# Kernel tuning notes

Measured on AMD Instinct MI355X. Metric: run time of the kernel, lower is better.

Reference implementation:

```python
import jax, jax.numpy as jnp
import numpy as np

NEG_SLOPE = 0.2  # PyG GATConv default negative_slope
EPS = 1e-16     # PyG softmax denominator epsilon


def gat_conv(x, src, dst, W, a_src, a_dst, bias):
    """PyG GATConv (concat=True, dropout off). x:[N,Fin], src/dst:[E]."""
    N = x.shape[0]
    H, C = a_src.shape
    h = (x @ W).reshape(N, H, C)                      # per-head projected features
    es = jnp.einsum('nhc,hc->nh', h, a_src)           # alpha_src per node/head
    ed = jnp.einsum('nhc,hc->nh', h, a_dst)           # alpha_dst per node/head
    e = jax.nn.leaky_relu(es[src] + ed[dst], NEG_SLOPE)   # [E,H] edge scores
    # segment softmax over destination nodes (every node has a self loop)
    m = jax.ops.segment_max(e, dst, num_segments=N)
    p = jnp.exp(e - m[dst])
    denom = jax.ops.segment_sum(p, dst, num_segments=N)
    alpha = p / (denom[dst] + EPS)                    # [E,H]
    out = jax.ops.segment_sum(h[src] * alpha[:, :, None], dst, num_segments=N)
    return out.reshape(N, H * C) + bias


def _single_graph(x, ei, W1, a_src1, a_dst1, b1, W2, a_src2, a_dst2, b2):
    N = x.shape[0]
    loop = jnp.arange(N, dtype=ei.dtype)              # add_self_loops=True
    src = jnp.concatenate([ei[0], loop])
    dst = jnp.concatenate([ei[1], loop])
    h = jax.nn.relu(gat_conv(x, src, dst, W1, a_src1, a_dst1, b1))
    # F.dropout with p=0.0 is identity
    return gat_conv(h, src, dst, W2, a_src2, a_dst2, b2)


def setup_inputs() -> dict:
    key = jax.random.key(0)
    ks = jax.random.split(key, 9)
    B, N, E, F_in, H, C = 2, 20000, 320000, 128, 8, 64

    def glorot(k, shape):
        fan_in, fan_out = shape[-2] if len(shape) > 1 else shape[-1], shape[-1]
        s = np.sqrt(6.0 / (fan_in + fan_out)).astype(np.float32)
        return jax.random.uniform(k, shape, jnp.float32, -s, s)

    return {
        'xs': jax.random.normal(ks[0], (B, N, F_in), jnp.float32),
        'edge_indexs': jax.random.randint(ks[1], (B, 2, E), 0, N, jnp.int32),
        'W1': glorot(ks[2], (F_in, H * C)),
        'a_src1': glorot(ks[3], (H, C)),
        'a_dst1': glorot(ks[4], (H, C)),
        'b1': jnp.zeros((H * C,), jnp.float32),
        'W2': glorot(ks[5], (H * C, C)),
        'a_src2': glorot(ks[6], (1, C)),
        'a_dst2': glorot(ks[7], (1, C)),
        'b2': jnp.zeros((C,), jnp.float32),
    }


def reference(xs, edge_indexs, W1, a_src1, a_dst1, b1, W2, a_src2, a_dst2, b2):
    f = lambda x, ei: _single_graph(x, ei, W1, a_src1, a_dst1, b1, W2, a_src2, a_dst2, b2)
    return jax.vmap(f)(xs, edge_indexs)               # [B, N, C]
```

## Files before the change

kernel.cpp:

```cpp
#include <hip/hip_runtime.h>
#include <hip/hip_bf16.h>
#include <cstdint>

#define NEG_SLOPE 0.2f
#define SOFTMAX_EPS 1e-16f
#define NN 20000
#define EE 320000
#define CAP 48

typedef __hip_bfloat16 bf16;
typedef unsigned short ushort;
typedef short s8v __attribute__((ext_vector_type(8)));
typedef float f4v __attribute__((ext_vector_type(4)));
typedef float f2v __attribute__((ext_vector_type(2)));

static __device__ __forceinline__ float lo16(unsigned u) { return __uint_as_float(u << 16); }
static __device__ __forceinline__ float hi16(unsigned u) { return __uint_as_float(u & 0xffff0000u); }
static __device__ __forceinline__ ushort f2bf(float v) {
    bf16 h = __float2bfloat16(v);
    return *(ushort*)&h;
}

__global__ void prep_kernel(const float* __restrict__ W1, const float* __restrict__ W2,
                            const float* __restrict__ xs,
                            ushort* __restrict__ w1hi, ushort* __restrict__ w1lo,
                            ushort* __restrict__ w2hi, ushort* __restrict__ w2lo,
                            ushort* __restrict__ xhi, ushort* __restrict__ xlo,
                            int* __restrict__ count) {
    int bid = blockIdx.x;
    int t = threadIdx.x;
    if (bid >= 205) {
        size_t idx = (size_t)(bid - 205) * 2048 + (size_t)t * 8;
        float4 A = *(const float4*)&xs[idx];
        float4 B = *(const float4*)&xs[idx + 4];
        float v[8] = {A.x, A.y, A.z, A.w, B.x, B.y, B.z, B.w};
        unsigned hp[4], lp[4];
#pragma unroll
        for (int p = 0; p < 4; ++p) {
            ushort h0 = f2bf(v[p * 2]), h1 = f2bf(v[p * 2 + 1]);
            float l0 = v[p * 2] - __uint_as_float((unsigned)h0 << 16);
            float l1 = v[p * 2 + 1] - __uint_as_float((unsigned)h1 << 16);
            hp[p] = (unsigned)h0 | ((unsigned)h1 << 16);
            lp[p] = (unsigned)f2bf(l0) | ((unsigned)f2bf(l1) << 16);
        }
        *(uint4*)&xhi[idx] = make_uint4(hp[0], hp[1], hp[2], hp[3]);
        *(uint4*)&xlo[idx] = make_uint4(lp[0], lp[1], lp[2], lp[3]);
        return;
    }
    if (bid >= 48) {
        int idx = (bid - 48) * 256 + t;
        if (idx < 2 * NN) count[idx] = 0;
        return;
    }
    __shared__ float T[32][65];
    const float* src; ushort *dhi, *dlo; int K, C, c0, k0;
    if (bid < 32) { src = W1; dhi = w1hi; dlo = w1lo; K = 128; C = 512; c0 = (bid & 7) * 64; k0 = (bid >> 3) * 32; }
    else          { src = W2; dhi = w2hi; dlo = w2lo; K = 512; C = 64;  c0 = 0;              k0 = (bid - 32) * 32; }
    for (int i = 0; i < 8; ++i) {
        int flat = t + i * 256;
        int k = flat >> 6, c = flat & 63;
        T[k][c] = src[(size_t)(k0 + k) * C + c0 + c];
    }
    __syncthreads();
    int c = t >> 2, j0 = (t & 3) * 8;
    unsigned hp[4], lp[4];
#pragma unroll
    for (int p = 0; p < 4; ++p) {
        float v0 = T[j0 + p * 2][c], v1 = T[j0 + p * 2 + 1][c];
        ushort h0 = f2bf(v0), h1 = f2bf(v1);
        float l0 = v0 - __uint_as_float((unsigned)h0 << 16);
        float l1 = v1 - __uint_as_float((unsigned)h1 << 16);
        hp[p] = (unsigned)h0 | ((unsigned)h1 << 16);
        lp[p] = (unsigned)f2bf(l0) | ((unsigned)f2bf(l1) << 16);
    }
    size_t o = (size_t)(c0 + c) * K + k0 + j0;
    *(uint4*)&dhi[o] = make_uint4(hp[0], hp[1], hp[2], hp[3]);
    *(uint4*)&dlo[o] = make_uint4(lp[0], lp[1], lp[2], lp[3]);
}

#define G1S 40
static __device__ void gemm1_body(int b, int rem,
        const ushort* __restrict__ xhi, const ushort* __restrict__ xlo,
        const ushort* __restrict__ w1hi, const ushort* __restrict__ w1lo,
        const float* __restrict__ a_src, const float* __restrict__ a_dst,
        bf16* __restrict__ h1, float* __restrict__ es, float* __restrict__ ed) {
    __shared__ ushort lds[25600];
    int t = threadIdx.x;
    ushort* Xhi = lds;
    ushort* Xlo = lds + 2560;
    ushort* Whi = lds + 5120;
    ushort* Wlo = lds + 15360;
    int w = t >> 6, lane = t & 63, quad = lane >> 4, l16 = lane & 15;
    int nhalf = rem / 313;
    int row0 = (rem % 313) * 64, nbase = nhalf * 256;
    const ushort* xh = xhi + (size_t)b * NN * 128;
    const ushort* xl = xlo + (size_t)b * NN * 128;
    bf16*  h1b = h1 + (size_t)b * NN * 512;
    float* esb = es + (size_t)b * NN * 8;
    float* edb = ed + (size_t)b * NN * 8;

    f4v acc[16];
#pragma unroll
    for (int i = 0; i < 16; ++i) acc[i] = (f4v)0.f;

    for (int kc = 0; kc < 4; ++kc) {
        __syncthreads();
        {
            int row = t >> 2, c0 = (t & 3) * 8;
            uint4 hv, lv;
            if (row0 + row < NN) {
                size_t off = (size_t)(row0 + row) * 128 + kc * 32 + c0;
                hv = *(const uint4*)&xh[off];
                lv = *(const uint4*)&xl[off];
            } else { hv = make_uint4(0, 0, 0, 0); lv = hv; }
            *(uint4*)&Xhi[row * G1S + c0] = hv;
            *(uint4*)&Xlo[row * G1S + c0] = lv;
        }
        {
            const ushort* sh = w1hi + (size_t)(nbase + t) * 128 + kc * 32;
            const ushort* sl = w1lo + (size_t)(nbase + t) * 128 + kc * 32;
            uint4 h0 = *(const uint4*)(sh), h1_ = *(const uint4*)(sh + 8);
            uint4 h2 = *(const uint4*)(sh + 16), h3 = *(const uint4*)(sh + 24);
            uint4 l0 = *(const uint4*)(sl), l1 = *(const uint4*)(sl + 8);
            uint4 l2 = *(const uint4*)(sl + 16), l3 = *(const uint4*)(sl + 24);
            *(uint4*)&Whi[t * G1S]      = h0; *(uint4*)&Whi[t * G1S + 8]  = h1_;
            *(uint4*)&Whi[t * G1S + 16] = h2; *(uint4*)&Whi[t * G1S + 24] = h3;
            *(uint4*)&Wlo[t * G1S]      = l0; *(uint4*)&Wlo[t * G1S + 8]  = l1;
            *(uint4*)&Wlo[t * G1S + 16] = l2; *(uint4*)&Wlo[t * G1S + 24] = l3;
        }
        __syncthreads();
        int arow = (w * 16 + l16) * G1S + quad * 8;
        s8v ahi = *(const s8v*)&Xhi[arow];
        s8v alo = *(const s8v*)&Xlo[arow];
#pragma unroll
        for (int ct = 0; ct < 16; ++ct) {
            int baddr = (ct * 16 + l16) * G1S + quad * 8;
            s8v bhi = *(const s8v*)&Whi[baddr];
            s8v blo = *(const s8v*)&Wlo[baddr];
            acc[ct] = __builtin_amdgcn_mfma_f32_16x16x32_bf16(ahi, bhi, acc[ct], 0, 0, 0);
            acc[ct] = __builtin_amdgcn_mfma_f32_16x16x32_bf16(ahi, blo, acc[ct], 0, 0, 0);
            acc[ct] = __builtin_amdgcn_mfma_f32_16x16x32_bf16(alo, bhi, acc[ct], 0, 0, 0);
        }
    }

#pragma unroll
    for (int hh = 0; hh < 4; ++hh) {
        float s4[4] = {0.f, 0.f, 0.f, 0.f}, d4[4] = {0.f, 0.f, 0.f, 0.f};
#pragma unroll
        for (int ct4 = 0; ct4 < 4; ++ct4) {
            int ct = hh * 4 + ct4;
            int c = nbase + ct * 16 + l16;
            float as = a_src[c], ad = a_dst[c];
#pragma unroll
            for (int r = 0; r < 4; ++r) { s4[r] += acc[ct][r] * as; d4[r] += acc[ct][r] * ad; }
        }
#pragma unroll
        for (int o = 1; o < 16; o <<= 1) {
#pragma unroll
            for (int r = 0; r < 4; ++r) {
                s4[r] += __shfl_xor(s4[r], o);
                d4[r] += __shfl_xor(d4[r], o);
            }
        }
        if (l16 == 0) {
            int head = nhalf * 4 + hh;
#pragma unroll
            for (int r = 0; r < 4; ++r) {
                int gr = row0 + w * 16 + quad * 4 + r;
                if (gr < NN) { esb[gr * 8 + head] = s4[r]; edb[gr * 8 + head] = d4[r]; }
            }
        }
    }

    __syncthreads();
    ushort* rp = lds + w * 4224;
#pragma unroll
    for (int ct = 0; ct < 16; ++ct)
#pragma unroll
        for (int r = 0; r < 4; ++r)
            rp[(quad * 4 + r) * 264 + ct * 16 + l16] = f2bf(acc[ct][r]);
#pragma unroll
    for (int i = 0; i < 8; ++i) {
        int idx = i * 512 + lane * 8;
        int row = idx >> 8, col = idx & 255;
        uint4 vv = *(const uint4*)&rp[row * 264 + col];
        int gr = row0 + w * 16 + row;
        if (gr < NN) *(uint4*)&h1b[(size_t)gr * 512 + nbase + col] = vv;
    }
}

static __device__ void scatter_body(int idx, const int* __restrict__ ei,
                                    int* __restrict__ count, ushort* __restrict__ esrc) {
    int t = threadIdx.x;
    int b = idx / 1250;
    int e = (idx % 1250) * 256 + t;
    const int* srcA = ei + (size_t)b * 2 * EE;
    int s = srcA[e], d = srcA[EE + e];
    if ((unsigned)d >= NN || (unsigned)s >= NN) return;
    int pos = atomicAdd(&count[b * NN + d], 1);
    if (pos < CAP)
        esrc[((size_t)b * NN + d) * CAP + pos] = (ushort)s;
}

__global__ __launch_bounds__(256) void gemm1_scatter(
        const ushort* __restrict__ xhi, const ushort* __restrict__ xlo,
        const ushort* __restrict__ w1hi, const ushort* __restrict__ w1lo,
        const float* __restrict__ a_src, const float* __restrict__ a_dst,
        bf16* __restrict__ h1, float* __restrict__ es, float* __restrict__ ed,
        const int* __restrict__ ei, int* __restrict__ count, ushort* __restrict__ esrc) {
    int bid = blockIdx.x;
    if (bid < 1252) gemm1_body(bid / 626, bid % 626, xhi, xlo, w1hi, w1lo, a_src, a_dst, h1, es, ed);
    else            scatter_body(bid - 1252, ei, count, esrc);
}

#define G2S 72
__global__ __launch_bounds__(256) void gemm2_mfma(
        const bf16* __restrict__ a, const ushort* __restrict__ w2hi,
        const ushort* __restrict__ w2lo, const float* __restrict__ a_src,
        const float* __restrict__ a_dst, bf16* __restrict__ h2,
        float* __restrict__ es, float* __restrict__ ed) {
    __shared__ ushort lds2[13824];
    ushort* AS  = lds2;
    ushort* Whi = lds2 + 4608;
    ushort* Wlo = lds2 + 9216;

    int t = threadIdx.x;
    int w = t >> 6, lane = t & 63, quad = lane >> 4, l16 = lane & 15;
    int b = blockIdx.y;
    int row0 = blockIdx.x * 64;
    const bf16* ab = a + (size_t)b * NN * 512;
    bf16*  h2b = h2 + (size_t)b * NN * 512;
    float* esb = es + (size_t)b * NN;
    float* edb = ed + (size_t)b * NN;

    f4v acc[4];
#pragma unroll
    for (int i = 0; i < 4; ++i) acc[i] = (f4v)0.f;

    for (int kc = 0; kc < 8; ++kc) {
        __syncthreads();
        {
            int row = t >> 2, k0 = (t & 3) * 16;
            uint4 q0, q1;
            if (row0 + row < NN) {
                q0 = *(const uint4*)(ab + (size_t)(row0 + row) * 512 + kc * 64 + k0);
                q1 = *(const uint4*)(ab + (size_t)(row0 + row) * 512 + kc * 64 + k0 + 8);
            } else { q0 = make_uint4(0, 0, 0, 0); q1 = q0; }
            *(uint4*)&AS[row * G2S + k0]     = q0;
            *(uint4*)&AS[row * G2S + k0 + 8] = q1;
            const ushort* sh = w2hi + (size_t)row * 512 + kc * 64 + k0;
            const ushort* sl = w2lo + (size_t)row * 512 + kc * 64 + k0;
            *(uint4*)&Whi[row * G2S + k0]     = *(const uint4*)(sh);
            *(uint4*)&Whi[row * G2S + k0 + 8] = *(const uint4*)(sh + 8);
            *(uint4*)&Wlo[row * G2S + k0]     = *(const uint4*)(sl);
            *(uint4*)&Wlo[row * G2S + k0 + 8] = *(const uint4*)(sl + 8);
        }
        __syncthreads();
#pragma unroll
        for (int ks = 0; ks < 2; ++ks) {
            s8v av = *(const s8v*)&AS[(w * 16 + l16) * G2S + ks * 32 + quad * 8];
#pragma unroll
            for (int ct = 0; ct < 4; ++ct) {
                int baddr = (ct * 16 + l16) * G2S + ks * 32 + quad * 8;
                s8v bhi = *(const s8v*)&Whi[baddr];
                s8v blo = *(const s8v*)&Wlo[baddr];
                acc[ct] = __builtin_amdgcn_mfma_f32_16x16x32_bf16(av, bhi, acc[ct], 0, 0, 0);
                acc[ct] = __builtin_amdgcn_mfma_f32_16x16x32_bf16(av, blo, acc[ct], 0, 0, 0);
            }
        }
    }

    {
        float s4[4] = {0.f, 0.f, 0.f, 0.f}, d4[4] = {0.f, 0.f, 0.f, 0.f};
#pragma unroll
        for (int ct = 0; ct < 4; ++ct) {
            int c = ct * 16 + l16;
            float as = a_src[c], ad = a_dst[c];
#pragma unroll
            for (int r = 0; r < 4; ++r) { s4[r] += acc[ct][r] * as; d4[r] += acc[ct][r] * ad; }
        }
#pragma unroll
        for (int o = 1; o < 16; o <<= 1) {
#pragma unroll
            for (int r = 0; r < 4; ++r) {
                s4[r] += __shfl_xor(s4[r], o);
                d4[r] += __shfl_xor(d4[r], o);
            }
        }
        if (l16 == 0) {
#pragma unroll
            for (int r = 0; r < 4; ++r) {
                int gr = row0 + w * 16 + quad * 4 + r;
                if (gr < NN) { esb[gr] = s4[r]; edb[gr] = d4[r]; }
            }
        }
    }

    __syncthreads();
    ushort* rp = lds2 + w * 1152;
#pragma unroll
    for (int ct = 0; ct < 4; ++ct)
#pragma unroll
        for (int r = 0; r < 4; ++r)
            rp[(quad * 4 + r) * G2S + ct * 16 + l16] = f2bf(acc[ct][r]);
#pragma unroll
    for (int i = 0; i < 2; ++i) {
        int idx = i * 512 + lane * 8;
        int row = idx >> 6, col = idx & 63;
        uint4 vv = *(const uint4*)&rp[row * G2S + col];
        int gr = row0 + w * 16 + row;
        if (gr < NN) *(uint4*)&h2b[(size_t)gr * 64 + col] = vv;
    }
}

__global__ __launch_bounds__(256) void aggregate1_kernel(int b,
        const bf16* __restrict__ h1, const float* __restrict__ es,
        const float* __restrict__ ed, const int* __restrict__ count,
        const ushort* __restrict__ esrc, const float* __restrict__ b1,
        bf16* __restrict__ out1) {
    __shared__ float alds[4][2][2][32];
    __shared__ unsigned offs[4][2][32];

    int t = threadIdx.x;
    int wv = t >> 6, lane = t & 63;
    int j = blockIdx.x;
    int qtr = (j & 7) >> 1;
    int qidx = (j >> 3) * 2 + (j & 1);
    int nA = qidx * 8 + wv * 2;
    int nd = lane >> 5;
    int slot = lane & 31;
    int n_lane = nA + nd;

    const bf16*  h1b = h1 + (size_t)b * NN * 512;
    const float* esb = es + (size_t)b * NN * 8;
    const float* edb = ed + (size_t)b * NN * 8;
    bf16* out1b = out1 + (size_t)b * NN * 512;

    int deg_e_lane = count[b * NN + n_lane];
    deg_e_lane = max(0, min(deg_e_lane, CAP));
    int degAe = __shfl(deg_e_lane, 0);
    int degBe = __shfl(deg_e_lane, 32);

    if (degAe > 31 || degBe > 31) {
        unsigned cb64 = (unsigned)qtr * 256u + (unsigned)lane * 4u;
        for (int k = 0; k < 2; ++k) {
            int nn = nA + k;
            int de = count[b * NN + nn];
            de = max(0, min(de, CAP));
            int dg = de + 1;
            bool act2 = lane < dg;
            int sr = act2 ? ((lane < de) ? (int)esrc[((size_t)b * NN + nn) * CAP + lane] : nn) : 0;
            float2 edv2 = *(const float2*)&edb[nn * 8 + qtr * 2];
            float2 esv2 = *(const float2*)((const char*)esb + ((unsigned)sr << 5) + (unsigned)qtr * 8u);
            float e0 = esv2.x + edv2.x; e0 = (e0 >= 0.f) ? e0 : NEG_SLOPE * e0; e0 = act2 ? e0 : -1e30f;
            float e1 = esv2.y + edv2.y; e1 = (e1 >= 0.f) ? e1 : NEG_SLOPE * e1; e1 = act2 ? e1 : -1e30f;
            float m0 = e0, m1 = e1;
#pragma unroll
            for (int o = 32; o > 0; o >>= 1) {
                m0 = fmaxf(m0, __shfl_xor(m0, o));
                m1 = fmaxf(m1, __shfl_xor(m1, o));
            }
            float p0 = act2 ? __expf(e0 - m0) : 0.f;
            float p1 = act2 ? __expf(e1 - m1) : 0.f;
            float s0 = p0, s1 = p1;
#pragma unroll
            for (int o = 32; o > 0; o >>= 1) {
                s0 += __shfl_xor(s0, o);
                s1 += __shfl_xor(s1, o);
            }
            float a0 = p0 / (s0 + SOFTMAX_EPS);
            float a1 = p1 / (s1 + SOFTMAX_EPS);
            f2v acc = {0.f, 0.f};
            for (int jj = 0; jj < dg; ++jj) {
                int sj = __shfl(sr, jj);
                float aw0 = __shfl(a0, jj);
                float aw1 = __shfl(a1, jj);
                float aw = (lane >= 32) ? aw1 : aw0;
                unsigned u = *(const unsigned*)((const char*)h1b + ((unsigned)sj << 10) + cb64);
                f2v tv = {lo16(u), hi16(u)};
                f2v wp2 = {aw, aw};
                acc += tv * wp2;
            }
            float2 bv2 = *(const float2*)&b1[qtr * 128 + lane * 2];
            union { ushort us[2]; unsigned u1; } pk;
            pk.us[0] = f2bf(fmaxf(acc.x + bv2.x, 0.f));
            pk.us[1] = f2bf(fmaxf(acc.y + bv2.y, 0.f));
            *(unsigned*)(out1b + (size_t)nn * 512 + qtr * 128 + lane * 2) = pk.u1;
        }
        return;
    }

    int deg = deg_e_lane + 1;
    bool act = slot < deg;
    size_t beg = ((size_t)b * NN + n_lane) * CAP;
    int sreg = act ? ((slot < deg_e_lane) ? (int)esrc[beg + slot] : n_lane) : 0;
    float2 edv = *(const float2*)&edb[n_lane * 8 + qtr * 2];
    float2 esv = *(const float2*)((const char*)esb + ((unsigned)sreg << 5) + (unsigned)qtr * 8u);
    float e0 = esv.x + edv.x; e0 = (e0 >= 0.f) ? e0 : NEG_SLOPE * e0; e0 = act ? e0 : -1e30f;
    float e1 = esv.y + edv.y; e1 = (e1 >= 0.f) ? e1 : NEG_SLOPE * e1; e1 = act ? e1 : -1e30f;
    float m0 = e0, m1 = e1;
#pragma unroll
    for (int o = 16; o > 0; o >>= 1) {
        m0 = fmaxf(m0, __shfl_xor(m0, o));
        m1 = fmaxf(m1, __shfl_xor(m1, o));
    }
    float p0 = act ? __expf(e0 - m0) : 0.f;
    float p1 = act ? __expf(e1 - m1) : 0.f;
    float s0 = p0, s1 = p1;
#pragma unroll
    for (int o = 16; o > 0; o >>= 1) {
        s0 += __shfl_xor(s0, o);
        s1 += __shfl_xor(s1, o);
    }
    offs[wv][nd][slot] = act ? ((unsigned)sreg << 10) : 0u;
    alds[wv][nd][0][slot] = p0 / (s0 + SOFTMAX_EPS);
    alds[wv][nd][1][slot] = p1 / (s1 + SOFTMAX_EPS);

    int mh = slot >> 4;
    const unsigned* op = &offs[wv][nd][0];
    const float*    wp = &alds[wv][nd][mh][0];
    unsigned cb = (unsigned)qtr * 256u + (unsigned)slot * 8u;
    uint64_t hbu = (uint64_t)(uintptr_t)h1b;
    unsigned hb_lo = __builtin_amdgcn_readfirstlane((unsigned)hbu);
    unsigned hb_hi = __builtin_amdgcn_readfirstlane((unsigned)(hbu >> 32));
    uint64_t hbs = ((uint64_t)hb_hi << 32) | (uint64_t)hb_lo;
    int mdeg = max(degAe, degBe) + 1;
    int trips = (mdeg + 3) >> 2;
    int trips2 = (trips + 1) & ~1;

    f2v acc0 = {0.f, 0.f}, acc1 = {0.f, 0.f};
    uint2 A0, A1, A2, A3, B0, B1, B2, B3;
    float4 wA, wB;

#define GLOAD(dst, voff) \
    asm volatile("global_load_dwordx2 %0, %1, %2" : "=&v"(dst) : "v"(voff), "s"(hbs))

#define LOADBANK(U0, U1, U2, U3, W4, blk) do { \
        int s_ = (blk) << 2; \
        uint4 ov_ = *(const uint4*)&op[s_]; \
        W4 = *(const float4*)&wp[s_]; \
        unsigned va_ = ov_.x + cb, vb_ = ov_.y + cb; \
        unsigned vc_ = ov_.z + cb, vd_ = ov_.w + cb; \
        GLOAD(U0, va_); GLOAD(U1, vb_); GLOAD(U2, vc_); GLOAD(U3, vd_); \
    } while (0)

#define WAITSB(nlit) do { \
        asm volatile("s_waitcnt vmcnt(" #nlit ")" ::: "memory"); \
        __builtin_amdgcn_sched_barrier(0); \
    } while (0)

#define ROW(U, W) do { \
        f2v wp_ = {W, W}; \
        f2v t0_ = {lo16(U.x), hi16(U.x)}; acc0 += t0_ * wp_; \
        f2v t1_ = {lo16(U.y), hi16(U.y)}; acc1 += t1_ * wp_; \
    } while (0)

#define CONSUME(U0, U1, U2, U3, W4) do { \
        ROW(U0, W4.x); ROW(U1, W4.y); ROW(U2, W4.z); ROW(U3, W4.w); \
    } while (0)

    LOADBANK(A0, A1, A2, A3, wA, 0);
    LOADBANK(B0, B1, B2, B3, wB, 1);
    for (int it = 0; it + 2 < trips2; it += 2) {
        WAITSB(4);
        CONSUME(A0, A1, A2, A3, wA); LOADBANK(A0, A1, A2, A3, wA, it + 2);
        WAITSB(4);
        CONSUME(B0, B1, B2, B3, wB); LOADBANK(B0, B1, B2, B3, wB, it + 3);
    }
    WAITSB(4);
    CONSUME(A0, A1, A2, A3, wA);
    WAITSB(0);
    CONSUME(B0, B1, B2, B3, wB);

#undef GLOAD
#undef LOADBANK
#undef WAITSB
#undef ROW
#undef CONSUME

    float4 bv = *(const float4*)&b1[qtr * 128 + slot * 4];
    union { ushort us[4]; uint2 u2; } pack;
    pack.us[0] = f2bf(fmaxf(acc0.x + bv.x, 0.f));
    pack.us[1] = f2bf(fmaxf(acc0.y + bv.y, 0.f));
    pack.us[2] = f2bf(fmaxf(acc1.x + bv.z, 0.f));
    pack.us[3] = f2bf(fmaxf(acc1.y + bv.w, 0.f));
    *(uint2*)(out1b + (size_t)n_lane * 512 + qtr * 128 + slot * 4) = pack.u2;
}

__global__ void aggregate2_kernel(const bf16* __restrict__ h2, const float* __restrict__ es,
                                  const float* __restrict__ ed, const int* __restrict__ count,
                                  const ushort* __restrict__ esrc, const float* __restrict__ bias2,
                                  float* __restrict__ out) {
    __shared__ float wl[4][64];
    __shared__ int slidx[4][64];
    int t = threadIdx.x;
    int wv = t >> 6, lane = t & 63;
    int bid = blockIdx.x;
    int xcd = bid & 7;
    int q = bid >> 3;
    int b = xcd >> 2;
    int n = (xcd & 3) * 5000 + q * 4 + wv;

    const bf16*  h2b = h2 + (size_t)b * NN * 512;
    const float* esb = es + (size_t)b * NN;
    const float* edb = ed + (size_t)b * NN;
    float* outb = out + (size_t)b * NN * 64;

    int deg_e = count[b * NN + n];
    deg_e = max(0, min(deg_e, CAP));
    int deg = deg_e + 1;
    size_t beg = ((size_t)b * NN + n) * CAP;
    float edn = edb[n];

    bool act = lane < deg;
    int sreg = act ? ((lane < deg_e) ? (int)esrc[beg + lane] : n) : 0;
    float ev = act ? esb[sreg] + edn : -1e30f;
    ev = (ev >= 0.f) ? ev : NEG_SLOPE * ev;
    if (!act) ev = -1e30f;
    float m = ev;
#pragma unroll
    for (int o = 32; o > 0; o >>= 1) m = fmaxf(m, __shfl_xor(m, o));
    float p = act ? __expf(ev - m) : 0.f;
    float sum = p;
#pragma unroll
    for (int o = 32; o > 0; o >>= 1) sum += __shfl_xor(sum, o);
    slidx[wv][lane] = sreg;
    wl[wv][lane] = p / (sum + SOFTMAX_EPS);

    float acc[4] = {0.f, 0.f, 0.f, 0.f};
    int grp = lane >> 4, ch4 = (lane & 15) * 4;
    int j = grp;
    for (; j + 4 < deg; j += 8) {
        int sA = slidx[wv][j];     float wA = wl[wv][j];
        int sB = slidx[wv][j + 4]; float wB = wl[wv][j + 4];
        uint2 uA = *(const uint2*)(h2b + (size_t)sA * 64 + ch4);
        uint2 uB = *(const uint2*)(h2b + (size_t)sB * 64 + ch4);
        acc[0] += wA * lo16(uA.x); acc[1] += wA * hi16(uA.x);
        acc[2] += wA * lo16(uA.y); acc[3] += wA * hi16(uA.y);
        acc[0] += wB * lo16(uB.x); acc[1] += wB * hi16(uB.x);
        acc[2] += wB * lo16(uB.y); acc[3] += wB * hi16(uB.y);
    }
    for (; j < deg; j += 4) {
        int s = slidx[wv][j];
        float wt = wl[wv][j];
        uint2 u = *(const uint2*)(h2b + (size_t)s * 64 + ch4);
        acc[0] += wt * lo16(u.x); acc[1] += wt * hi16(u.x);
        acc[2] += wt * lo16(u.y); acc[3] += wt * hi16(u.y);
    }
#pragma unroll
    for (int i = 0; i < 4; ++i) {
        acc[i] += __shfl_xor(acc[i], 16);
        acc[i] += __shfl_xor(acc[i], 32);
    }
    if (lane < 16) {
        float4 o4;
        o4.x = acc[0] + bias2[ch4 + 0];
        o4.y = acc[1] + bias2[ch4 + 1];
        o4.z = acc[2] + bias2[ch4 + 2];
        o4.w = acc[3] + bias2[ch4 + 3];
        *(float4*)&outb[(size_t)n * 64 + ch4] = o4;
    }
}

extern "C" void kernel_launch(void* const* d_in, const int* in_sizes, int n_in,
                              void* d_out, int out_size, void* d_ws, size_t ws_size,
                              hipStream_t stream) {
    const float* xs     = (const float*)d_in[0];
    const int*   ei     = (const int*)d_in[1];
    const float* W1     = (const float*)d_in[2];
    const float* a_src1 = (const float*)d_in[3];
    const float* a_dst1 = (const float*)d_in[4];
    const float* b1     = (const float*)d_in[5];
    const float* W2     = (const float*)d_in[6];
    const float* a_src2 = (const float*)d_in[7];
    const float* a_dst2 = (const float*)d_in[8];
    const float* b2     = (const float*)d_in[9];
    float* out = (float*)d_out;

    const int B = 2;

    uintptr_t p = (uintptr_t)d_ws;
    auto alloc = [&](size_t bytes) {
        void* r = (void*)p;
        p += (bytes + 255) & ~(size_t)255;
        return r;
    };
    bf16* h1   = (bf16*)alloc((size_t)B * NN * 512 * 2);
    bf16* out1 = (bf16*)alloc((size_t)B * NN * 512 * 2);
    char* unionA = (char*)alloc((size_t)B * NN * 64 * 2);
    float*  es1   = (float*)unionA;
    float*  ed1   = (float*)(unionA + 1280000);
    ushort* wt1hi = (ushort*)(unionA + 2560000);
    ushort* wt1lo = (ushort*)(unionA + 2560000 + 131072);
    bf16*   h2    = h1;
    ushort* xhi   = (ushort*)out1;
    ushort* xlo   = xhi + (size_t)B * NN * 128;
    ushort* wt2hi = (ushort*)alloc((size_t)64 * 512 * 2);
    ushort* wt2lo = (ushort*)alloc((size_t)64 * 512 * 2);
    float* es2    = (float*)alloc((size_t)B * NN * 4);
    float* ed2    = (float*)alloc((size_t)B * NN * 4);
    int*   count  = (int*)alloc((size_t)B * NN * 4);
    ushort* esrc  = (ushort*)alloc((size_t)B * NN * CAP * 2);

    prep_kernel<<<2705, 256, 0, stream>>>(W1, W2, xs, wt1hi, wt1lo, wt2hi, wt2lo,
                                          xhi, xlo, count);
    gemm1_scatter<<<1252 + 2500, 256, 0, stream>>>(xhi, xlo, wt1hi, wt1lo, a_src1, a_dst1,
                                                   h1, es1, ed1, ei, count, esrc);
    aggregate1_kernel<<<10000, 256, 0, stream>>>(0, h1, es1, ed1, count, esrc, b1, out1);
    aggregate1_kernel<<<10000, 256, 0, stream>>>(1, h1, es1, ed1, count, esrc, b1, out1);
    gemm2_mfma<<<dim3(313, B), 256, 0, stream>>>(out1, wt2hi, wt2lo, a_src2, a_dst2, h2, es2, ed2);
    aggregate2_kernel<<<10000, 256, 0, stream>>>(h2, es2, ed2, count, esrc, b2, out);
}
```

Before: 279.5 us.

## Halve GEMM1 column tile and merge both aggregate1 batch launches into one

```diff
diff --git a/kernel.cpp b/kernel.cpp
--- a/kernel.cpp
+++ b/kernel.cpp
@@ -84,24 +84,24 @@
         const ushort* __restrict__ w1hi, const ushort* __restrict__ w1lo,
         const float* __restrict__ a_src, const float* __restrict__ a_dst,
         bf16* __restrict__ h1, float* __restrict__ es, float* __restrict__ ed) {
-    __shared__ ushort lds[25600];
+    __shared__ ushort lds[15360];
     int t = threadIdx.x;
     ushort* Xhi = lds;
     ushort* Xlo = lds + 2560;
     ushort* Whi = lds + 5120;
-    ushort* Wlo = lds + 15360;
+    ushort* Wlo = lds + 10240;
     int w = t >> 6, lane = t & 63, quad = lane >> 4, l16 = lane & 15;
-    int nhalf = rem / 313;
-    int row0 = (rem % 313) * 64, nbase = nhalf * 256;
+    int nq = rem / 313;
+    int row0 = (rem % 313) * 64, nbase = nq * 128;
     const ushort* xh = xhi + (size_t)b * NN * 128;
     const ushort* xl = xlo + (size_t)b * NN * 128;
     bf16*  h1b = h1 + (size_t)b * NN * 512;
     float* esb = es + (size_t)b * NN * 8;
     float* edb = ed + (size_t)b * NN * 8;
 
-    f4v acc[16];
-#pragma unroll
-    for (int i = 0; i < 16; ++i) acc[i] = (f4v)0.f;
+    f4v acc[8];
+#pragma unroll
+    for (int i = 0; i < 8; ++i) acc[i] = (f4v)0.f;
 
     for (int kc = 0; kc < 4; ++kc) {
         __syncthreads();
@@ -117,23 +117,22 @@
             *(uint4*)&Xlo[row * G1S + c0] = lv;
         }
         {
-            const ushort* sh = w1hi + (size_t)(nbase + t) * 128 + kc * 32;
-            const ushort* sl = w1lo + (size_t)(nbase + t) * 128 + kc * 32;
+            int c = t >> 1, k0 = (t & 1) * 16;
+            const ushort* sh = w1hi + (size_t)(nbase + c) * 128 + kc * 32 + k0;
+            const ushort* sl = w1lo + (size_t)(nbase + c) * 128 + kc * 32 + k0;
             uint4 h0 = *(const uint4*)(sh), h1_ = *(const uint4*)(sh + 8);
-            uint4 h2 = *(const uint4*)(sh + 16), h3 = *(const uint4*)(sh + 24);
-            uint4 l0 = *(const uint4*)(sl), l1 = *(const uint4*)(sl + 8);
-            uint4 l2 = *(const uint4*)(sl + 16), l3 = *(const uint4*)(sl + 24);
-            *(uint4*)&Whi[t * G1S]      = h0; *(uint4*)&Whi[t * G1S + 8]  = h1_;
-            *(uint4*)&Whi[t * G1S + 16] = h2; *(uint4*)&Whi[t * G1S + 24] = h3;
-            *(uint4*)&Wlo[t * G1S]      = l0; *(uint4*)&Wlo[t * G1S + 8]  = l1;
-            *(uint4*)&Wlo[t * G1S + 16] = l2; *(uint4*)&Wlo[t * G1S + 24] = l3;
+            uint4 l0 = *(const uint4*)(sl), l1_ = *(const uint4*)(sl + 8);
+            *(uint4*)&Whi[c * G1S + k0]     = h0;
+            *(uint4*)&Whi[c * G1S + k0 + 8] = h1_;
+            *(uint4*)&Wlo[c * G1S + k0]     = l0;
+            *(uint4*)&Wlo[c * G1S + k0 + 8] = l1_;
         }
         __syncthreads();
         int arow = (w * 16 + l16) * G1S + quad * 8;
         s8v ahi = *(const s8v*)&Xhi[arow];
         s8v alo = *(const s8v*)&Xlo[arow];
 #pragma unroll
-        for (int ct = 0; ct < 16; ++ct) {
+        for (int ct = 0; ct < 8; ++ct) {
             int baddr = (ct * 16 + l16) * G1S + quad * 8;
             s8v bhi = *(const s8v*)&Whi[baddr];
             s8v blo = *(const s8v*)&Wlo[baddr];
@@ -144,7 +143,7 @@
     }
 
 #pragma unroll
-    for (int hh = 0; hh < 4; ++hh) {
+    for (int hh = 0; hh < 2; ++hh) {
         float s4[4] = {0.f, 0.f, 0.f, 0.f}, d4[4] = {0.f, 0.f, 0.f, 0.f};
 #pragma unroll
         for (int ct4 = 0; ct4 < 4; ++ct4) {
@@ -163,7 +162,7 @@
             }
         }
         if (l16 == 0) {
-            int head = nhalf * 4 + hh;
+            int head = nq * 2 + hh;
 #pragma unroll
             for (int r = 0; r < 4; ++r) {
                 int gr = row0 + w * 16 + quad * 4 + r;
@@ -173,17 +172,17 @@
     }
 
     __syncthreads();
-    ushort* rp = lds + w * 4224;
-#pragma unroll
-    for (int ct = 0; ct < 16; ++ct)
+    ushort* rp = lds + w * 2176;
+#pragma unroll
+    for (int ct = 0; ct < 8; ++ct)
 #pragma unroll
         for (int r = 0; r < 4; ++r)
-            rp[(quad * 4 + r) * 264 + ct * 16 + l16] = f2bf(acc[ct][r]);
-#pragma unroll
-    for (int i = 0; i < 8; ++i) {
+            rp[(quad * 4 + r) * 136 + ct * 16 + l16] = f2bf(acc[ct][r]);
+#pragma unroll
+    for (int i = 0; i < 4; ++i) {
         int idx = i * 512 + lane * 8;
-        int row = idx >> 8, col = idx & 255;
-        uint4 vv = *(const uint4*)&rp[row * 264 + col];
+        int row = idx >> 7, col = idx & 127;
+        uint4 vv = *(const uint4*)&rp[row * 136 + col];
         int gr = row0 + w * 16 + row;
         if (gr < NN) *(uint4*)&h1b[(size_t)gr * 512 + nbase + col] = vv;
     }
@@ -209,8 +208,8 @@
         bf16* __restrict__ h1, float* __restrict__ es, float* __restrict__ ed,
         const int* __restrict__ ei, int* __restrict__ count, ushort* __restrict__ esrc) {
     int bid = blockIdx.x;
-    if (bid < 1252) gemm1_body(bid / 626, bid % 626, xhi, xlo, w1hi, w1lo, a_src, a_dst, h1, es, ed);
-    else            scatter_body(bid - 1252, ei, count, esrc);
+    if (bid < 2504) gemm1_body(bid / 1252, bid % 1252, xhi, xlo, w1hi, w1lo, a_src, a_dst, h1, es, ed);
+    else            scatter_body(bid - 2504, ei, count, esrc);
 }
 
 #define G2S 72
@@ -313,7 +312,7 @@
     }
 }
 
-__global__ __launch_bounds__(256) void aggregate1_kernel(int b,
+__global__ __launch_bounds__(256) void aggregate1_kernel(
         const bf16* __restrict__ h1, const float* __restrict__ es,
         const float* __restrict__ ed, const int* __restrict__ count,
         const ushort* __restrict__ esrc, const float* __restrict__ b1,
@@ -323,10 +322,11 @@
 
     int t = threadIdx.x;
     int wv = t >> 6, lane = t & 63;
-    int j = blockIdx.x;
-    int qtr = (j & 7) >> 1;
-    int qidx = (j >> 3) * 2 + (j & 1);
-    int nA = qidx * 8 + wv * 2;
+    int bid = blockIdx.x;
+    int combo = bid & 7;
+    int b = combo >> 2;
+    int qtr = combo & 3;
+    int nA = (bid >> 3) * 8 + wv * 2;
     int nd = lane >> 5;
     int slot = lane & 31;
     int n_lane = nA + nd;
@@ -604,10 +604,9 @@
 
     prep_kernel<<<2705, 256, 0, stream>>>(W1, W2, xs, wt1hi, wt1lo, wt2hi, wt2lo,
                                           xhi, xlo, count);
-    gemm1_scatter<<<1252 + 2500, 256, 0, stream>>>(xhi, xlo, wt1hi, wt1lo, a_src1, a_dst1,
+    gemm1_scatter<<<2504 + 2500, 256, 0, stream>>>(xhi, xlo, wt1hi, wt1lo, a_src1, a_dst1,
                                                    h1, es1, ed1, ei, count, esrc);
-    aggregate1_kernel<<<10000, 256, 0, stream>>>(0, h1, es1, ed1, count, esrc, b1, out1);
-    aggregate1_kernel<<<10000, 256, 0, stream>>>(1, h1, es1, ed1, count, esrc, b1, out1);
+    aggregate1_kernel<<<20000, 256, 0, stream>>>(h1, es1, ed1, count, esrc, b1, out1);
     gemm2_mfma<<<dim3(313, B), 256, 0, stream>>>(out1, wt2hi, wt2lo, a_src2, a_dst2, h2, es2, ed2);
     aggregate2_kernel<<<10000, 256, 0, stream>>>(h2, es2, ed2, count, esrc, b2, out);
 }
```

Result: faster. 272.9 us (-2.4%).
